# Performance work log

Hardware: AMD Instinct MI355X
Metric: run time of the kernel (lower is better)

## Reference

```python
import jax, jax.numpy as jnp
import numpy as np

N = 30000   # fluid particles
E = 480000  # edges
F = 4       # fluidFeatures (in channels)
P = 8       # RBF basis size per dim (dims=[8], 1D)
LAYERS = [32, 64, 64, 2]


def hat_basis(x, n):
    # 'linear' RBF: hat functions on n evenly spaced centers in [-1, 1]
    centers = jnp.linspace(-1.0, 1.0, n, dtype=x.dtype)
    spacing = 2.0 / (n - 1)
    return jnp.maximum(0.0, 1.0 - jnp.abs(x[:, None] - centers[None, :]) / spacing)  # [E, n]


def rbf_conv(x, fi, fj, d, W, b, mask, n_nodes):
    # x: [N, Cin]; d: [E, 1] clamped; W: [P, Cin, Cout]; b: [Cout]
    phi = hat_basis(d[:, 0], W.shape[0])      # [E, P]
    xj = x[fj]                                 # gather source features [E, Cin]
    msg = jnp.zeros((xj.shape[0], W.shape[2]), dtype=x.dtype)
    for p in range(W.shape[0]):                # small fixed P=8 loop keeps memory O(E*Cout)
        msg = msg + phi[:, p, None] * (xj @ W[p])
    msg = jnp.where(mask[:, None], msg, 0.0)   # centerIgnore: drop self edges fi==fj
    out = jax.ops.segment_sum(msg, fi, num_segments=n_nodes)  # scatter-reduce to targets
    return out + b


def _xavier(key, shape_in, shape_out):
    lim = float(np.sqrt(6.0 / (shape_in + shape_out)))
    return jax.random.uniform(key, (shape_in, shape_out), jnp.float32, -lim, lim)


def setup_inputs() -> dict:
    key = jax.random.key(0)
    ks = jax.random.split(key, 16)
    fluidFeatures = jax.random.normal(ks[0], (N, F), jnp.float32)
    fi = jax.random.randint(ks[1], (E,), 0, N)
    fj = jax.random.randint(ks[2], (E,), 0, N)
    distances = jax.random.normal(ks[3], (E, 1), jnp.float32)
    # conv channels: 4->32, 64->64, 64->64, 64->2
    cio = [(F, 32), (2 * 32, 64), (64, 64), (64, 2)]
    inp = {"fluidFeatures": fluidFeatures, "fi": fi, "fj": fj, "distances": distances}
    for li, (ci, co) in enumerate(cio):
        inp[f"cW{li}"] = jax.random.normal(ks[4 + li], (P, ci, co), jnp.float32) * (1.0 / np.sqrt(P * ci))
        inp[f"cb{li}"] = jnp.zeros((co,), jnp.float32)
        inp[f"fW{li}"] = _xavier(ks[8 + li], ci, co)   # stored [in, out]
        inp[f"fb{li}"] = jnp.zeros((co,), jnp.float32)
    return inp


def reference(fluidFeatures, fi, fj, distances,
              cW0, cb0, fW0, fb0, cW1, cb1, fW1, fb1,
              cW2, cb2, fW2, fb2, cW3, cb3, fW3, fb3):
    n_nodes = fluidFeatures.shape[0]
    mask = fi != fj                     # centerIgnore (mask instead of filter: jit-safe)
    d = jnp.clip(distances, -1.0, 1.0)

    conv0 = rbf_conv(fluidFeatures, fi, fj, d, cW0, cb0, mask, n_nodes)  # [N, 32]
    lin0 = fluidFeatures @ fW0 + fb0                                      # [N, 32]
    ans = jnp.concatenate([lin0, conv0], axis=1)                          # [N, 64]

    # i = 1: features[0]=32 != features[1]=64 -> no residual
    ansc = jax.nn.relu(ans)
    ans = rbf_conv(ansc, fi, fj, d, cW1, cb1, mask, n_nodes) + (ansc @ fW1 + fb1)
    # i = 2: features[1]==features[2]==64 and shapes match -> residual
    ansc = jax.nn.relu(ans)
    ans = rbf_conv(ansc, fi, fj, d, cW2, cb2, mask, n_nodes) + (ansc @ fW2 + fb2) + ans
    # i = 3: 64 -> 2, no residual
    ansc = jax.nn.relu(ans)
    ans = rbf_conv(ansc, fi, fj, d, cW3, cb3, mask, n_nodes) + (ansc @ fW3 + fb3)

    return ans  # dim == 1 (dims=[8]) -> no /128
```

## Files before the change

### kernel.cpp

```cpp
#include <hip/hip_runtime.h>


#define CAP 48

typedef __attribute__((ext_vector_type(8))) short short8;
typedef __attribute__((ext_vector_type(4))) short short4v;
typedef __attribute__((ext_vector_type(4))) float f32x4;

__device__ __forceinline__ short bf16s(float f) {
  unsigned u = __float_as_uint(f);
  return (short)((u + 0x7FFF + ((u >> 16) & 1)) >> 16);
}
__device__ __forceinline__ float b2f(unsigned short s) {
  return __uint_as_float(((unsigned)s) << 16);
}

__global__ void fill_prep(const float* __restrict__ dist,
                          const int* __restrict__ fi, const int* __restrict__ fj,
                          int* __restrict__ cnt, int* __restrict__ jw, int nE,
                          const float* __restrict__ cW1, const float* __restrict__ fW1,
                          const float* __restrict__ cW2, const float* __restrict__ fW2,
                          short* __restrict__ wt1, short* __restrict__ wt2,
                          int fillBlocks) {
  if ((int)blockIdx.x < fillBlocks) {
    int e = blockIdx.x * blockDim.x + threadIdx.x;
    if (e >= nE) return;
    int i = fi[e], j = fj[e];
    if (i == j) return;
    float d = fminf(1.0f, fmaxf(-1.0f, dist[e]));
    float u = (d + 1.0f) * 3.5f;
    int p = min((int)u, 6);
    float w0 = 1.0f - (u - (float)p);
    int wq = (int)(w0 * 16383.0f + 0.5f);
    int pos = atomicAdd(&cnt[i], 1);
    if (pos < CAP)
      jw[(size_t)i * CAP + pos] = j | (p << 15) | (wq << 18);
  } else {
    int idx = ((int)blockIdx.x - fillBlocks) * blockDim.x + threadIdx.x;
    if (idx >= 2 * 576 * 64) return;
    int sel = idx / (576 * 64);
    int r = idx - sel * (576 * 64);
    int col = r >> 6, ch = r & 63;
    const float* cW = sel ? cW2 : cW1;
    const float* fW = sel ? fW2 : fW1;
    float v;
    if (col < 512) {
      int p = col >> 6, co = col & 63;
      v = cW[((size_t)p * 64 + ch) * 64 + co];
    } else {
      v = fW[(size_t)ch * 64 + (col - 512)];
    }
    (sel ? wt2 : wt1)[(size_t)col * 64 + ch] = bf16s(v);
  }
}

__global__ __launch_bounds__(256) void layer0_kernel(
    const float* __restrict__ X,
    const int* __restrict__ cnt, const int* __restrict__ jw,
    const float* __restrict__ cW0,
    const float* __restrict__ cb0,
    const float* __restrict__ fW0,
    const float* __restrict__ fb0,
    unsigned short* __restrict__ ansc0, int n) {
  __shared__ float sW[1024];
  __shared__ float sF[128];
  __shared__ float sB[64];
  __shared__ float sacc[4][32];
  for (int idx = threadIdx.x; idx < 1024; idx += 256) sW[idx] = cW0[idx];
  for (int idx = threadIdx.x; idx < 128; idx += 256) sF[idx] = fW0[idx];
  if (threadIdx.x < 32) sB[threadIdx.x] = cb0[threadIdx.x];
  else if (threadIdx.x < 64) sB[threadIdx.x] = fb0[threadIdx.x - 32];
  const int w = threadIdx.x >> 6;
  const int lane = threadIdx.x & 63;
  const int i = blockIdx.x * 4 + w;
  const bool valid = (i < n);
  if (valid && lane < 32) sacc[w][lane] = 0.0f;
  __syncthreads();
  if (valid && lane < min(cnt[i], CAP)) {
    int v = jw[(size_t)i * CAP + lane];
    int j = v & 0x7FFF;
    int p = (v >> 15) & 7;
    float w0 = (float)((unsigned)v >> 18) * (1.0f / 16383.0f);
    float w1 = 1.0f - w0;
    float4 x = *(const float4*)(X + (size_t)j * 4);
    atomicAdd(&sacc[w][p * 4 + 0], w0 * x.x);
    atomicAdd(&sacc[w][p * 4 + 1], w0 * x.y);
    atomicAdd(&sacc[w][p * 4 + 2], w0 * x.z);
    atomicAdd(&sacc[w][p * 4 + 3], w0 * x.w);
    atomicAdd(&sacc[w][(p + 1) * 4 + 0], w1 * x.x);
    atomicAdd(&sacc[w][(p + 1) * 4 + 1], w1 * x.y);
    atomicAdd(&sacc[w][(p + 1) * 4 + 2], w1 * x.z);
    atomicAdd(&sacc[w][(p + 1) * 4 + 3], w1 * x.w);
  }
  __syncthreads();
  if (!valid) return;
  const float4 xi = *(const float4*)(X + (size_t)i * 4);
  float v;
  if (lane < 32) {
    v = sB[32 + lane];
    v = fmaf(xi.x, sF[0 * 32 + lane], v);
    v = fmaf(xi.y, sF[1 * 32 + lane], v);
    v = fmaf(xi.z, sF[2 * 32 + lane], v);
    v = fmaf(xi.w, sF[3 * 32 + lane], v);
  } else {
    const int cc = lane - 32;
    v = sB[cc];
    #pragma unroll
    for (int k = 0; k < 32; ++k)
      v = fmaf(sacc[w][k], sW[k * 32 + cc], v);
  }
  ansc0[(size_t)i * 64 + lane] = (unsigned short)bf16s(fmaxf(v, 0.0f));
}

__global__ __launch_bounds__(256) void gemm_ul(
    const unsigned short* __restrict__ Xb,
    const short* __restrict__ WTul,
    unsigned short* __restrict__ UL, int n) {
  __shared__ short sUL[16 * 584];
  const int lane = threadIdx.x & 63;
  const int w = threadIdx.x >> 6;
  const int mrow = lane & 15;
  const int quad = lane >> 4;
  const int nodeBase = blockIdx.x * 16;
  const int bnode = min(nodeBase + mrow, n - 1);
  const unsigned short* bBase = Xb + (size_t)bnode * 64 + quad * 8;
  short8 b0 = *(const short8*)(bBase);
  short8 b1 = *(const short8*)(bBase + 32);
  #pragma unroll
  for (int t = 0; t < 9; ++t) {
    const int ct = w * 9 + t;
    const short* aBase = WTul + (size_t)(ct * 16 + mrow) * 64 + quad * 8;
    short8 a0 = *(const short8*)(aBase);
    short8 a1 = *(const short8*)(aBase + 32);
    f32x4 acc = {0, 0, 0, 0};
    acc = __builtin_amdgcn_mfma_f32_16x16x32_bf16(a0, b0, acc, 0, 0, 0);
    acc = __builtin_amdgcn_mfma_f32_16x16x32_bf16(a1, b1, acc, 0, 0, 0);
    short4v pk;
    #pragma unroll
    for (int reg = 0; reg < 4; ++reg) pk[reg] = bf16s(acc[reg]);
    *(short4v*)(sUL + mrow * 584 + ct * 16 + quad * 4) = pk;
  }
  __syncthreads();
  const int r = threadIdx.x >> 4;
  const int c0 = threadIdx.x & 15;
  if (nodeBase + r < n) {
    unsigned short* dst = UL + (size_t)(nodeBase + r) * 576;
    #pragma unroll
    for (int chunk = c0; chunk < 72; chunk += 16)
      *(short8*)(dst + chunk * 8) = *(const short8*)(sUL + r * 584 + chunk * 8);
  }
}

template <bool HAS_RES, bool STORE_ANS, bool COMPUTE_T>
__global__ __launch_bounds__(256) void conv_gather(
    const unsigned short* __restrict__ UL,
    const int* __restrict__ cnt, const int* __restrict__ jw,
    const float* __restrict__ cb, const float* __restrict__ fb,
    const float* __restrict__ resid,
    const float* __restrict__ cW3,
    float* __restrict__ T,
    float* __restrict__ outAns,
    unsigned short* __restrict__ outAnsc, int n) {
  const int lane = threadIdx.x & 63;
  const int half = lane >> 5;
  const int pl = lane & 31;
  const int i = (blockIdx.x * blockDim.x + threadIdx.x) >> 6;
  if (i >= n) return;
  int rec = jw[(size_t)i * CAP + (lane < CAP ? lane : 0)];
  const int m = min(cnt[i], CAP);
  const unsigned short* ULrow = UL + (size_t)i * 576;
  const unsigned Lraw = ((const unsigned*)(ULrow + 512))[pl];
  float rv0 = 0.0f, rv1 = 0.0f;
  if (HAS_RES) {
    float2 rv = *(const float2*)(resid + (size_t)i * 64 + 2 * pl);
    rv0 = rv.x; rv1 = rv.y;
  }
  float accLo = 0.0f, accHi = 0.0f;
  for (int q0 = 0; q0 < m; q0 += 16) {
    unsigned raw[16];
    float w0s[16];
    #pragma unroll
    for (int k = 0; k < 16; ++k) {
      int v = __builtin_amdgcn_readlane(rec, q0 + k);
      int j = min(v & 0x7FFF, n - 1);
      int p = (v >> 15) & 7;
      w0s[k] = (float)((unsigned)v >> 18) * (1.0f / 16383.0f);
      raw[k] = ((const unsigned*)(UL + (size_t)j * 576 + p * 64))[lane];
    }
    #pragma unroll
    for (int k = 0; k < 16; ++k) {
      bool ok = (q0 + k < m);
      float w = half ? (1.0f - w0s[k]) : w0s[k];
      w = ok ? w : 0.0f;
      float lo = __uint_as_float(raw[k] << 16);
      float hi = __uint_as_float(raw[k] & 0xFFFF0000u);
      accLo = fmaf(w, lo, accLo);
      accHi = fmaf(w, hi, accHi);
    }
  }
  accLo += __shfl_xor(accLo, 32, 64);
  accHi += __shfl_xor(accHi, 32, 64);
  if (half == 0) {
    const int c0i = 2 * pl, c1i = c0i + 1;
    float L0 = __uint_as_float(Lraw << 16);
    float L1 = __uint_as_float(Lraw & 0xFFFF0000u);
    float o0 = accLo + L0 + cb[c0i] + fb[c0i] + rv0;
    float o1 = accHi + L1 + cb[c1i] + fb[c1i] + rv1;
    if (STORE_ANS)
      *(float2*)(outAns + (size_t)i * 64 + c0i) = make_float2(o0, o1);
    unsigned short xb0 = (unsigned short)bf16s(fmaxf(o0, 0.0f));
    unsigned short xb1 = (unsigned short)bf16s(fmaxf(o1, 0.0f));
    ((unsigned*)(outAnsc + (size_t)i * 64))[pl] = (unsigned)xb0 | ((unsigned)xb1 << 16);
    if (COMPUTE_T) {
      float x0 = b2f(xb0), x1 = b2f(xb1);
      float c[16];
      #pragma unroll
      for (int t = 0; t < 16; ++t) {
        const float* wrow = cW3 + ((size_t)(t >> 1) * 64) * 2 + (t & 1);
        c[t] = x0 * wrow[c0i * 2] + x1 * wrow[c1i * 2];
      }
      #pragma unroll
      for (int off = 16; off > 0; off >>= 1) {
        #pragma unroll
        for (int t = 0; t < 16; ++t) c[t] += __shfl_xor(c[t], off, 64);
      }
      if (pl == 0) {
        float* tr = T + (size_t)i * 16;
        #pragma unroll
        for (int t = 0; t < 16; ++t) tr[t] = c[t];
      }
    }
  }
}

__global__ __launch_bounds__(256, 4) void layer3_kernel(
    const unsigned short* __restrict__ Xb,
    const float* __restrict__ T,
    const int* __restrict__ cnt, const int* __restrict__ jw,
    const float* __restrict__ cb3, const float* __restrict__ fb3,
    const float* __restrict__ fW3,
    float* __restrict__ out, int n) {
  const int lane = threadIdx.x & 63;
  const int i = (blockIdx.x * blockDim.x + threadIdx.x) >> 6;
  if (i >= n) return;
  const int m = min(cnt[i], CAP);
  float c0 = 0.0f, c1 = 0.0f;
  if (lane < m) {
    int v = jw[(size_t)i * CAP + lane];
    int j = min(v & 0x7FFF, n - 1);
    int p = (v >> 15) & 7;
    float w0 = (float)((unsigned)v >> 18) * (1.0f / 16383.0f);
    float w1 = 1.0f - w0;
    const float* tb = T + (size_t)j * 16 + p * 2;
    float2 ta = *(const float2*)(tb);
    float2 tc = *(const float2*)(tb + 2);
    c0 = w0 * ta.x + w1 * tc.x;
    c1 = w0 * ta.y + w1 * tc.y;
  }
  float xi = b2f(Xb[(size_t)i * 64 + lane]);
  float2 fw = *(const float2*)(fW3 + lane * 2);
  c0 = fmaf(xi, fw.x, c0);
  c1 = fmaf(xi, fw.y, c1);
  #pragma unroll
  for (int off = 32; off > 0; off >>= 1) {
    c0 += __shfl_xor(c0, off, 64);
    c1 += __shfl_xor(c1, off, 64);
  }
  if (lane == 0) {
    out[(size_t)i * 2 + 0] = c0 + cb3[0] + fb3[0];
    out[(size_t)i * 2 + 1] = c1 + cb3[1] + fb3[1];
  }
}

extern "C" void kernel_launch(void* const* d_in, const int* in_sizes, int n_in,
                              void* d_out, int out_size, void* d_ws, size_t ws_size,
                              hipStream_t stream) {
  const float* X    = (const float*)d_in[0];
  const int*   fi   = (const int*)d_in[1];
  const int*   fj   = (const int*)d_in[2];
  const float* dist = (const float*)d_in[3];
  const float* cW0 = (const float*)d_in[4];  const float* cb0 = (const float*)d_in[5];
  const float* fW0 = (const float*)d_in[6];  const float* fb0 = (const float*)d_in[7];
  const float* cW1 = (const float*)d_in[8];  const float* cb1 = (const float*)d_in[9];
  const float* fW1 = (const float*)d_in[10]; const float* fb1 = (const float*)d_in[11];
  const float* cW2 = (const float*)d_in[12]; const float* cb2 = (const float*)d_in[13];
  const float* fW2 = (const float*)d_in[14]; const float* fb2 = (const float*)d_in[15];
  const float* cW3 = (const float*)d_in[16]; const float* cb3 = (const float*)d_in[17];
  const float* fW3 = (const float*)d_in[18]; const float* fb3 = (const float*)d_in[19];
  float* out = (float*)d_out;

  const int n  = in_sizes[0] / 4;
  const int nE = in_sizes[1];

  unsigned short* UL    = (unsigned short*)d_ws;
  unsigned short* ansc0 = UL + (size_t)n * 576;
  unsigned short* ansc1 = ansc0 + (size_t)n * 64;
  float*          ans1  = (float*)(ansc1 + (size_t)n * 64);
  unsigned short* ansc2 = ansc0;
  float* T     = ans1 + (size_t)n * 64;
  short* wtul1 = (short*)(T + (size_t)n * 16);
  short* wtul2 = wtul1 + 576 * 64;
  int*   jw    = (int*)(wtul2 + 576 * 64);
  int*   cnt   = jw + (size_t)n * CAP;

  hipMemsetAsync(cnt, 0, (size_t)n * sizeof(int), stream);
  const int fillBlocks = (nE + 255) / 256;
  const int prepBlocks = (2 * 576 * 64 + 255) / 256;
  fill_prep<<<fillBlocks + prepBlocks, 256, 0, stream>>>(
      dist, fi, fj, cnt, jw, nE, cW1, fW1, cW2, fW2, wtul1, wtul2, fillBlocks);

  layer0_kernel<<<(n + 3) / 4, 256, 0, stream>>>(X, cnt, jw,
                                                 cW0, cb0, fW0, fb0, ansc0, n);
  gemm_ul<<<(n + 15) / 16, 256, 0, stream>>>(ansc0, wtul1, UL, n);
  conv_gather<false, true, false><<<(n * 64 + 255) / 256, 256, 0, stream>>>(
      UL, cnt, jw, cb1, fb1, nullptr, nullptr, nullptr, ans1, ansc1, n);
  gemm_ul<<<(n + 15) / 16, 256, 0, stream>>>(ansc1, wtul2, UL, n);
  conv_gather<true, false, true><<<(n * 64 + 255) / 256, 256, 0, stream>>>(
      UL, cnt, jw, cb2, fb2, ans1, cW3, T, nullptr, ansc2, n);
  layer3_kernel<<<(n * 64 + 255) / 256, 256, 0, stream>>>(ansc2, T, cnt, jw,
                                                          cb3, fb3, fW3, out, n);
}
```

Measured before the change: 270.2 us.

## Fuse all stages into one persistent cooperative kernel with grid syncs

Replaces the memset and the six separate kernel launches with a single cooperative persistent kernel. It iterates over nodes and tiles with grid-stride loops and separates the phases with grid.sync(). This removes per-launch overhead and the memset. In exchange it adds grid-wide barrier costs, lowers occupancy through the fixed block count, and calls hipGetDeviceProperties and the occupancy query on every launch.

```diff
diff --git a/kernel.cpp b/kernel.cpp
--- a/kernel.cpp
+++ b/kernel.cpp
@@ -1,4 +1,7 @@
 #include <hip/hip_runtime.h>
+#include <hip/hip_cooperative_groups.h>
+
+namespace cg = cooperative_groups;
 
 
 #define CAP 48
@@ -15,34 +18,153 @@
   return __uint_as_float(((unsigned)s) << 16);
 }
 
-__global__ void fill_prep(const float* __restrict__ dist,
-                          const int* __restrict__ fi, const int* __restrict__ fj,
-                          int* __restrict__ cnt, int* __restrict__ jw, int nE,
-                          const float* __restrict__ cW1, const float* __restrict__ fW1,
-                          const float* __restrict__ cW2, const float* __restrict__ fW2,
-                          short* __restrict__ wt1, short* __restrict__ wt2,
-                          int fillBlocks) {
-  if ((int)blockIdx.x < fillBlocks) {
-    int e = blockIdx.x * blockDim.x + threadIdx.x;
-    if (e >= nE) return;
-    int i = fi[e], j = fj[e];
-    if (i == j) return;
-    float d = fminf(1.0f, fmaxf(-1.0f, dist[e]));
-    float u = (d + 1.0f) * 3.5f;
-    int p = min((int)u, 6);
-    float w0 = 1.0f - (u - (float)p);
-    int wq = (int)(w0 * 16383.0f + 0.5f);
-    int pos = atomicAdd(&cnt[i], 1);
-    if (pos < CAP)
-      jw[(size_t)i * CAP + pos] = j | (p << 15) | (wq << 18);
-  } else {
-    int idx = ((int)blockIdx.x - fillBlocks) * blockDim.x + threadIdx.x;
-    if (idx >= 2 * 576 * 64) return;
+struct MegaParams {
+  const float* X; const int* fi; const int* fj; const float* dist;
+  const float* cW0; const float* cb0; const float* fW0; const float* fb0;
+  const float* cW1; const float* cb1; const float* fW1; const float* fb1;
+  const float* cW2; const float* cb2; const float* fW2; const float* fb2;
+  const float* cW3; const float* cb3; const float* fW3; const float* fb3;
+  unsigned short* UL; unsigned short* ansc0; unsigned short* ansc1;
+  float* ans1; float* T; short* wt1; short* wt2; int* jw; int* cnt;
+  float* out; int n; int nE;
+};
+
+__device__ __forceinline__ void gemm_ul_phase(
+    const unsigned short* __restrict__ Xb, const short* __restrict__ WTul,
+    unsigned short* __restrict__ UL, int n, char* smemRaw) {
+  short* sUL = (short*)smemRaw;
+  const int lane = threadIdx.x & 63;
+  const int w = threadIdx.x >> 6;
+  const int mrow = lane & 15;
+  const int quad = lane >> 4;
+  for (int tile = blockIdx.x; tile * 16 < n; tile += gridDim.x) {
+    __syncthreads();
+    const int nodeBase = tile * 16;
+    const int bnode = min(nodeBase + mrow, n - 1);
+    const unsigned short* bBase = Xb + (size_t)bnode * 64 + quad * 8;
+    short8 b0 = *(const short8*)(bBase);
+    short8 b1 = *(const short8*)(bBase + 32);
+    #pragma unroll
+    for (int t = 0; t < 9; ++t) {
+      const int ct = w * 9 + t;
+      const short* aBase = WTul + (size_t)(ct * 16 + mrow) * 64 + quad * 8;
+      short8 a0 = *(const short8*)(aBase);
+      short8 a1 = *(const short8*)(aBase + 32);
+      f32x4 acc = {0, 0, 0, 0};
+      acc = __builtin_amdgcn_mfma_f32_16x16x32_bf16(a0, b0, acc, 0, 0, 0);
+      acc = __builtin_amdgcn_mfma_f32_16x16x32_bf16(a1, b1, acc, 0, 0, 0);
+      short4v pk;
+      #pragma unroll
+      for (int reg = 0; reg < 4; ++reg) pk[reg] = bf16s(acc[reg]);
+      *(short4v*)(sUL + mrow * 584 + ct * 16 + quad * 4) = pk;
+    }
+    __syncthreads();
+    const int r = threadIdx.x >> 4;
+    const int c0 = threadIdx.x & 15;
+    if (nodeBase + r < n) {
+      unsigned short* dst = UL + (size_t)(nodeBase + r) * 576;
+      #pragma unroll
+      for (int chunk = c0; chunk < 72; chunk += 16)
+        *(short8*)(dst + chunk * 8) = *(const short8*)(sUL + r * 584 + chunk * 8);
+    }
+  }
+}
+
+template <bool HAS_RES, bool STORE_ANS, bool COMPUTE_T>
+__device__ __forceinline__ void conv_phase(
+    const unsigned short* __restrict__ UL,
+    const int* __restrict__ cnt, const int* __restrict__ jw,
+    const float* __restrict__ cb, const float* __restrict__ fb,
+    const float* __restrict__ resid, const float* __restrict__ cW3,
+    float* __restrict__ T, float* __restrict__ outAns,
+    unsigned short* __restrict__ outAnsc, int n, int gwave, int NW) {
+  const int lane = threadIdx.x & 63;
+  const int half = lane >> 5;
+  const int pl = lane & 31;
+  const int c0i = 2 * pl, c1i = c0i + 1;
+  const float cbf0 = cb[c0i] + fb[c0i];
+  const float cbf1 = cb[c1i] + fb[c1i];
+  for (int i = gwave; i < n; i += NW) {
+    int rec = jw[(size_t)i * CAP + (lane < CAP ? lane : 0)];
+    const int m = min(cnt[i], CAP);
+    const unsigned Lraw = ((const unsigned*)(UL + (size_t)i * 576 + 512))[pl];
+    float rv0 = 0.0f, rv1 = 0.0f;
+    if (HAS_RES) {
+      float2 rv = *(const float2*)(resid + (size_t)i * 64 + 2 * pl);
+      rv0 = rv.x; rv1 = rv.y;
+    }
+    float accLo = 0.0f, accHi = 0.0f;
+    for (int q0 = 0; q0 < m; q0 += 16) {
+      unsigned raw[16];
+      float w0s[16];
+      #pragma unroll
+      for (int k = 0; k < 16; ++k) {
+        int v = __builtin_amdgcn_readlane(rec, q0 + k);
+        int j = min(v & 0x7FFF, n - 1);
+        int p = (v >> 15) & 7;
+        w0s[k] = (float)((unsigned)v >> 18) * (1.0f / 16383.0f);
+        raw[k] = ((const unsigned*)(UL + (size_t)j * 576 + p * 64))[lane];
+      }
+      #pragma unroll
+      for (int k = 0; k < 16; ++k) {
+        bool ok = (q0 + k < m);
+        float w = half ? (1.0f - w0s[k]) : w0s[k];
+        w = ok ? w : 0.0f;
+        accLo = fmaf(w, __uint_as_float(raw[k] << 16), accLo);
+        accHi = fmaf(w, __uint_as_float(raw[k] & 0xFFFF0000u), accHi);
+      }
+    }
+    accLo += __shfl_xor(accLo, 32, 64);
+    accHi += __shfl_xor(accHi, 32, 64);
+    if (half == 0) {
+      float o0 = accLo + __uint_as_float(Lraw << 16) + cbf0 + rv0;
+      float o1 = accHi + __uint_as_float(Lraw & 0xFFFF0000u) + cbf1 + rv1;
+      if (STORE_ANS)
+        *(float2*)(outAns + (size_t)i * 64 + c0i) = make_float2(o0, o1);
+      unsigned short xb0 = (unsigned short)bf16s(fmaxf(o0, 0.0f));
+      unsigned short xb1 = (unsigned short)bf16s(fmaxf(o1, 0.0f));
+      ((unsigned*)(outAnsc + (size_t)i * 64))[pl] = (unsigned)xb0 | ((unsigned)xb1 << 16);
+      if (COMPUTE_T) {
+        float x0 = b2f(xb0), x1 = b2f(xb1);
+        float c[16];
+        #pragma unroll
+        for (int t = 0; t < 16; ++t) {
+          const float* wrow = cW3 + ((size_t)(t >> 1) * 64) * 2 + (t & 1);
+          c[t] = x0 * wrow[c0i * 2] + x1 * wrow[c1i * 2];
+        }
+        #pragma unroll
+        for (int off = 16; off > 0; off >>= 1) {
+          #pragma unroll
+          for (int t = 0; t < 16; ++t) c[t] += __shfl_xor(c[t], off, 64);
+        }
+        if (pl == 0) {
+          float* tr = T + (size_t)i * 16;
+          #pragma unroll
+          for (int t = 0; t < 16; ++t) tr[t] = c[t];
+        }
+      }
+    }
+  }
+}
+
+__global__ __launch_bounds__(256, 4) void mega_kernel(MegaParams P) {
+  cg::grid_group grid = cg::this_grid();
+  __shared__ __align__(16) char smem[18688];
+  const int tid = (int)(blockIdx.x * blockDim.x + threadIdx.x);
+  const int NT = (int)(gridDim.x * blockDim.x);
+  const int lane = threadIdx.x & 63;
+  const int wIn = threadIdx.x >> 6;
+  const int gwave = tid >> 6;
+  const int NW = NT >> 6;
+  const int n = P.n;
+
+  for (int i = tid; i < n; i += NT) P.cnt[i] = 0;
+  for (int idx = tid; idx < 2 * 576 * 64; idx += NT) {
     int sel = idx / (576 * 64);
     int r = idx - sel * (576 * 64);
     int col = r >> 6, ch = r & 63;
-    const float* cW = sel ? cW2 : cW1;
-    const float* fW = sel ? fW2 : fW1;
+    const float* cW = sel ? P.cW2 : P.cW1;
+    const float* fW = sel ? P.fW2 : P.fW1;
     float v;
     if (col < 512) {
       int p = col >> 6, co = col & 63;
@@ -50,273 +172,174 @@
     } else {
       v = fW[(size_t)ch * 64 + (col - 512)];
     }
-    (sel ? wt2 : wt1)[(size_t)col * 64 + ch] = bf16s(v);
-  }
-}
-
-__global__ __launch_bounds__(256) void layer0_kernel(
-    const float* __restrict__ X,
-    const int* __restrict__ cnt, const int* __restrict__ jw,
-    const float* __restrict__ cW0,
-    const float* __restrict__ cb0,
-    const float* __restrict__ fW0,
-    const float* __restrict__ fb0,
-    unsigned short* __restrict__ ansc0, int n) {
-  __shared__ float sW[1024];
-  __shared__ float sF[128];
-  __shared__ float sB[64];
-  __shared__ float sacc[4][32];
-  for (int idx = threadIdx.x; idx < 1024; idx += 256) sW[idx] = cW0[idx];
-  for (int idx = threadIdx.x; idx < 128; idx += 256) sF[idx] = fW0[idx];
-  if (threadIdx.x < 32) sB[threadIdx.x] = cb0[threadIdx.x];
-  else if (threadIdx.x < 64) sB[threadIdx.x] = fb0[threadIdx.x - 32];
-  const int w = threadIdx.x >> 6;
-  const int lane = threadIdx.x & 63;
-  const int i = blockIdx.x * 4 + w;
-  const bool valid = (i < n);
-  if (valid && lane < 32) sacc[w][lane] = 0.0f;
-  __syncthreads();
-  if (valid && lane < min(cnt[i], CAP)) {
-    int v = jw[(size_t)i * CAP + lane];
-    int j = v & 0x7FFF;
-    int p = (v >> 15) & 7;
-    float w0 = (float)((unsigned)v >> 18) * (1.0f / 16383.0f);
-    float w1 = 1.0f - w0;
-    float4 x = *(const float4*)(X + (size_t)j * 4);
-    atomicAdd(&sacc[w][p * 4 + 0], w0 * x.x);
-    atomicAdd(&sacc[w][p * 4 + 1], w0 * x.y);
-    atomicAdd(&sacc[w][p * 4 + 2], w0 * x.z);
-    atomicAdd(&sacc[w][p * 4 + 3], w0 * x.w);
-    atomicAdd(&sacc[w][(p + 1) * 4 + 0], w1 * x.x);
-    atomicAdd(&sacc[w][(p + 1) * 4 + 1], w1 * x.y);
-    atomicAdd(&sacc[w][(p + 1) * 4 + 2], w1 * x.z);
-    atomicAdd(&sacc[w][(p + 1) * 4 + 3], w1 * x.w);
-  }
-  __syncthreads();
-  if (!valid) return;
-  const float4 xi = *(const float4*)(X + (size_t)i * 4);
-  float v;
-  if (lane < 32) {
-    v = sB[32 + lane];
-    v = fmaf(xi.x, sF[0 * 32 + lane], v);
-    v = fmaf(xi.y, sF[1 * 32 + lane], v);
-    v = fmaf(xi.z, sF[2 * 32 + lane], v);
-    v = fmaf(xi.w, sF[3 * 32 + lane], v);
-  } else {
-    const int cc = lane - 32;
-    v = sB[cc];
-    #pragma unroll
-    for (int k = 0; k < 32; ++k)
-      v = fmaf(sacc[w][k], sW[k * 32 + cc], v);
-  }
-  ansc0[(size_t)i * 64 + lane] = (unsigned short)bf16s(fmaxf(v, 0.0f));
-}
-
-__global__ __launch_bounds__(256) void gemm_ul(
-    const unsigned short* __restrict__ Xb,
-    const short* __restrict__ WTul,
-    unsigned short* __restrict__ UL, int n) {
-  __shared__ short sUL[16 * 584];
-  const int lane = threadIdx.x & 63;
-  const int w = threadIdx.x >> 6;
-  const int mrow = lane & 15;
-  const int quad = lane >> 4;
-  const int nodeBase = blockIdx.x * 16;
-  const int bnode = min(nodeBase + mrow, n - 1);
-  const unsigned short* bBase = Xb + (size_t)bnode * 64 + quad * 8;
-  short8 b0 = *(const short8*)(bBase);
-  short8 b1 = *(const short8*)(bBase + 32);
-  #pragma unroll
-  for (int t = 0; t < 9; ++t) {
-    const int ct = w * 9 + t;
-    const short* aBase = WTul + (size_t)(ct * 16 + mrow) * 64 + quad * 8;
-    short8 a0 = *(const short8*)(aBase);
-    short8 a1 = *(const short8*)(aBase + 32);
-    f32x4 acc = {0, 0, 0, 0};
-    acc = __builtin_amdgcn_mfma_f32_16x16x32_bf16(a0, b0, acc, 0, 0, 0);
-    acc = __builtin_amdgcn_mfma_f32_16x16x32_bf16(a1, b1, acc, 0, 0, 0);
-    short4v pk;
-    #pragma unroll
-    for (int reg = 0; reg < 4; ++reg) pk[reg] = bf16s(acc[reg]);
-    *(short4v*)(sUL + mrow * 584 + ct * 16 + quad * 4) = pk;
-  }
-  __syncthreads();
-  const int r = threadIdx.x >> 4;
-  const int c0 = threadIdx.x & 15;
-  if (nodeBase + r < n) {
-    unsigned short* dst = UL + (size_t)(nodeBase + r) * 576;
-    #pragma unroll
-    for (int chunk = c0; chunk < 72; chunk += 16)
-      *(short8*)(dst + chunk * 8) = *(const short8*)(sUL + r * 584 + chunk * 8);
-  }
-}
-
-template <bool HAS_RES, bool STORE_ANS, bool COMPUTE_T>
-__global__ __launch_bounds__(256) void conv_gather(
-    const unsigned short* __restrict__ UL,
-    const int* __restrict__ cnt, const int* __restrict__ jw,
-    const float* __restrict__ cb, const float* __restrict__ fb,
-    const float* __restrict__ resid,
-    const float* __restrict__ cW3,
-    float* __restrict__ T,
-    float* __restrict__ outAns,
-    unsigned short* __restrict__ outAnsc, int n) {
-  const int lane = threadIdx.x & 63;
-  const int half = lane >> 5;
-  const int pl = lane & 31;
-  const int i = (blockIdx.x * blockDim.x + threadIdx.x) >> 6;
-  if (i >= n) return;
-  int rec = jw[(size_t)i * CAP + (lane < CAP ? lane : 0)];
-  const int m = min(cnt[i], CAP);
-  const unsigned short* ULrow = UL + (size_t)i * 576;
-  const unsigned Lraw = ((const unsigned*)(ULrow + 512))[pl];
-  float rv0 = 0.0f, rv1 = 0.0f;
-  if (HAS_RES) {
-    float2 rv = *(const float2*)(resid + (size_t)i * 64 + 2 * pl);
-    rv0 = rv.x; rv1 = rv.y;
-  }
-  float accLo = 0.0f, accHi = 0.0f;
-  for (int q0 = 0; q0 < m; q0 += 16) {
-    unsigned raw[16];
-    float w0s[16];
-    #pragma unroll
-    for (int k = 0; k < 16; ++k) {
-      int v = __builtin_amdgcn_readlane(rec, q0 + k);
-      int j = min(v & 0x7FFF, n - 1);
-      int p = (v >> 15) & 7;
-      w0s[k] = (float)((unsigned)v >> 18) * (1.0f / 16383.0f);
-      raw[k] = ((const unsigned*)(UL + (size_t)j * 576 + p * 64))[lane];
-    }
-    #pragma unroll
-    for (int k = 0; k < 16; ++k) {
-      bool ok = (q0 + k < m);
-      float w = half ? (1.0f - w0s[k]) : w0s[k];
-      w = ok ? w : 0.0f;
-      float lo = __uint_as_float(raw[k] << 16);
-      float hi = __uint_as_float(raw[k] & 0xFFFF0000u);
-      accLo = fmaf(w, lo, accLo);
-      accHi = fmaf(w, hi, accHi);
-    }
-  }
-  accLo += __shfl_xor(accLo, 32, 64);
-  accHi += __shfl_xor(accHi, 32, 64);
-  if (half == 0) {
-    const int c0i = 2 * pl, c1i = c0i + 1;
-    float L0 = __uint_as_float(Lraw << 16);
-    float L1 = __uint_as_float(Lraw & 0xFFFF0000u);
-    float o0 = accLo + L0 + cb[c0i] + fb[c0i] + rv0;
-    float o1 = accHi + L1 + cb[c1i] + fb[c1i] + rv1;
-    if (STORE_ANS)
-      *(float2*)(outAns + (size_t)i * 64 + c0i) = make_float2(o0, o1);
-    unsigned short xb0 = (unsigned short)bf16s(fmaxf(o0, 0.0f));
-    unsigned short xb1 = (unsigned short)bf16s(fmaxf(o1, 0.0f));
-    ((unsigned*)(outAnsc + (size_t)i * 64))[pl] = (unsigned)xb0 | ((unsigned)xb1 << 16);
-    if (COMPUTE_T) {
-      float x0 = b2f(xb0), x1 = b2f(xb1);
-      float c[16];
-      #pragma unroll
-      for (int t = 0; t < 16; ++t) {
-        const float* wrow = cW3 + ((size_t)(t >> 1) * 64) * 2 + (t & 1);
-        c[t] = x0 * wrow[c0i * 2] + x1 * wrow[c1i * 2];
-      }
-      #pragma unroll
-      for (int off = 16; off > 0; off >>= 1) {
-        #pragma unroll
-        for (int t = 0; t < 16; ++t) c[t] += __shfl_xor(c[t], off, 64);
-      }
-      if (pl == 0) {
-        float* tr = T + (size_t)i * 16;
-        #pragma unroll
-        for (int t = 0; t < 16; ++t) tr[t] = c[t];
-      }
-    }
-  }
-}
-
-__global__ __launch_bounds__(256, 4) void layer3_kernel(
-    const unsigned short* __restrict__ Xb,
-    const float* __restrict__ T,
-    const int* __restrict__ cnt, const int* __restrict__ jw,
-    const float* __restrict__ cb3, const float* __restrict__ fb3,
-    const float* __restrict__ fW3,
-    float* __restrict__ out, int n) {
-  const int lane = threadIdx.x & 63;
-  const int i = (blockIdx.x * blockDim.x + threadIdx.x) >> 6;
-  if (i >= n) return;
-  const int m = min(cnt[i], CAP);
-  float c0 = 0.0f, c1 = 0.0f;
-  if (lane < m) {
-    int v = jw[(size_t)i * CAP + lane];
-    int j = min(v & 0x7FFF, n - 1);
-    int p = (v >> 15) & 7;
-    float w0 = (float)((unsigned)v >> 18) * (1.0f / 16383.0f);
-    float w1 = 1.0f - w0;
-    const float* tb = T + (size_t)j * 16 + p * 2;
-    float2 ta = *(const float2*)(tb);
-    float2 tc = *(const float2*)(tb + 2);
-    c0 = w0 * ta.x + w1 * tc.x;
-    c1 = w0 * ta.y + w1 * tc.y;
-  }
-  float xi = b2f(Xb[(size_t)i * 64 + lane]);
-  float2 fw = *(const float2*)(fW3 + lane * 2);
-  c0 = fmaf(xi, fw.x, c0);
-  c1 = fmaf(xi, fw.y, c1);
-  #pragma unroll
-  for (int off = 32; off > 0; off >>= 1) {
-    c0 += __shfl_xor(c0, off, 64);
-    c1 += __shfl_xor(c1, off, 64);
-  }
-  if (lane == 0) {
-    out[(size_t)i * 2 + 0] = c0 + cb3[0] + fb3[0];
-    out[(size_t)i * 2 + 1] = c1 + cb3[1] + fb3[1];
+    (sel ? P.wt2 : P.wt1)[(size_t)col * 64 + ch] = bf16s(v);
+  }
+  grid.sync();
+
+  for (int e = tid; e < P.nE; e += NT) {
+    int i = P.fi[e], j = P.fj[e];
+    if (i == j) continue;
+    float d = fminf(1.0f, fmaxf(-1.0f, P.dist[e]));
+    float u = (d + 1.0f) * 3.5f;
+    int p = min((int)u, 6);
+    float w0 = 1.0f - (u - (float)p);
+    int wq = (int)(w0 * 16383.0f + 0.5f);
+    int pos = atomicAdd(&P.cnt[i], 1);
+    if (pos < CAP)
+      P.jw[(size_t)i * CAP + pos] = j | (p << 15) | (wq << 18);
+  }
+  grid.sync();
+
+  {
+    float* sW = (float*)smem;
+    float* sF = sW + 1024;
+    float* sB = sF + 128;
+    float* sacc = sB + 64;
+    for (int idx = threadIdx.x; idx < 1024; idx += 256) sW[idx] = P.cW0[idx];
+    for (int idx = threadIdx.x; idx < 128; idx += 256) sF[idx] = P.fW0[idx];
+    if (threadIdx.x < 32) sB[threadIdx.x] = P.cb0[threadIdx.x];
+    else if (threadIdx.x < 64) sB[threadIdx.x] = P.fb0[threadIdx.x - 32];
+    for (int g4 = blockIdx.x; g4 * 4 < n; g4 += gridDim.x) {
+      const int i = g4 * 4 + wIn;
+      const bool valid = (i < n);
+      __syncthreads();
+      if (valid && lane < 32) sacc[wIn * 32 + lane] = 0.0f;
+      __syncthreads();
+      if (valid && lane < min(P.cnt[i], CAP)) {
+        int v = P.jw[(size_t)i * CAP + lane];
+        int j = v & 0x7FFF;
+        int p = (v >> 15) & 7;
+        float w0 = (float)((unsigned)v >> 18) * (1.0f / 16383.0f);
+        float w1 = 1.0f - w0;
+        float4 x = *(const float4*)(P.X + (size_t)j * 4);
+        atomicAdd(&sacc[wIn * 32 + p * 4 + 0], w0 * x.x);
+        atomicAdd(&sacc[wIn * 32 + p * 4 + 1], w0 * x.y);
+        atomicAdd(&sacc[wIn * 32 + p * 4 + 2], w0 * x.z);
+        atomicAdd(&sacc[wIn * 32 + p * 4 + 3], w0 * x.w);
+        atomicAdd(&sacc[wIn * 32 + (p + 1) * 4 + 0], w1 * x.x);
+        atomicAdd(&sacc[wIn * 32 + (p + 1) * 4 + 1], w1 * x.y);
+        atomicAdd(&sacc[wIn * 32 + (p + 1) * 4 + 2], w1 * x.z);
+        atomicAdd(&sacc[wIn * 32 + (p + 1) * 4 + 3], w1 * x.w);
+      }
+      __syncthreads();
+      if (valid) {
+        const float4 xi = *(const float4*)(P.X + (size_t)i * 4);
+        float v;
+        if (lane < 32) {
+          v = sB[32 + lane];
+          v = fmaf(xi.x, sF[0 * 32 + lane], v);
+          v = fmaf(xi.y, sF[1 * 32 + lane], v);
+          v = fmaf(xi.z, sF[2 * 32 + lane], v);
+          v = fmaf(xi.w, sF[3 * 32 + lane], v);
+        } else {
+          const int cc = lane - 32;
+          v = sB[cc];
+          #pragma unroll
+          for (int k = 0; k < 32; ++k)
+            v = fmaf(sacc[wIn * 32 + k], sW[k * 32 + cc], v);
+        }
+        P.ansc0[(size_t)i * 64 + lane] = (unsigned short)bf16s(fmaxf(v, 0.0f));
+      }
+    }
+  }
+  grid.sync();
+
+  gemm_ul_phase(P.ansc0, P.wt1, P.UL, n, smem);
+  grid.sync();
+  conv_phase<false, true, false>(P.UL, P.cnt, P.jw, P.cb1, P.fb1,
+                                 nullptr, nullptr, nullptr,
+                                 P.ans1, P.ansc1, n, gwave, NW);
+  grid.sync();
+  gemm_ul_phase(P.ansc1, P.wt2, P.UL, n, smem);
+  grid.sync();
+  conv_phase<true, false, true>(P.UL, P.cnt, P.jw, P.cb2, P.fb2,
+                                P.ans1, P.cW3, P.T,
+                                nullptr, P.ansc0, n, gwave, NW);
+  grid.sync();
+  {
+    const unsigned short* Xb = P.ansc0;
+    const float b3s0 = P.cb3[0] + P.fb3[0];
+    const float b3s1 = P.cb3[1] + P.fb3[1];
+    const float2 fw = *(const float2*)(P.fW3 + lane * 2);
+    for (int i = gwave; i < n; i += NW) {
+      const int m = min(P.cnt[i], CAP);
+      float c0 = 0.0f, c1 = 0.0f;
+      if (lane < m) {
+        int v = P.jw[(size_t)i * CAP + lane];
+        int j = min(v & 0x7FFF, n - 1);
+        int p = (v >> 15) & 7;
+        float w0 = (float)((unsigned)v >> 18) * (1.0f / 16383.0f);
+        float w1 = 1.0f - w0;
+        const float* tb = P.T + (size_t)j * 16 + p * 2;
+        float2 ta = *(const float2*)(tb);
+        float2 tc = *(const float2*)(tb + 2);
+        c0 = w0 * ta.x + w1 * tc.x;
+        c1 = w0 * ta.y + w1 * tc.y;
+      }
+      float xi = b2f(Xb[(size_t)i * 64 + lane]);
+      c0 = fmaf(xi, fw.x, c0);
+      c1 = fmaf(xi, fw.y, c1);
+      #pragma unroll
+      for (int off = 32; off > 0; off >>= 1) {
+        c0 += __shfl_xor(c0, off, 64);
+        c1 += __shfl_xor(c1, off, 64);
+      }
+      if (lane == 0) {
+        P.out[(size_t)i * 2 + 0] = c0 + b3s0;
+        P.out[(size_t)i * 2 + 1] = c1 + b3s1;
+      }
+    }
   }
 }
 
 extern "C" void kernel_launch(void* const* d_in, const int* in_sizes, int n_in,
                               void* d_out, int out_size, void* d_ws, size_t ws_size,
                               hipStream_t stream) {
-  const float* X    = (const float*)d_in[0];
-  const int*   fi   = (const int*)d_in[1];
-  const int*   fj   = (const int*)d_in[2];
-  const float* dist = (const float*)d_in[3];
-  const float* cW0 = (const float*)d_in[4];  const float* cb0 = (const float*)d_in[5];
-  const float* fW0 = (const float*)d_in[6];  const float* fb0 = (const float*)d_in[7];
-  const float* cW1 = (const float*)d_in[8];  const float* cb1 = (const float*)d_in[9];
-  const float* fW1 = (const float*)d_in[10]; const float* fb1 = (const float*)d_in[11];
-  const float* cW2 = (const float*)d_in[12]; const float* cb2 = (const float*)d_in[13];
-  const float* fW2 = (const float*)d_in[14]; const float* fb2 = (const float*)d_in[15];
-  const float* cW3 = (const float*)d_in[16]; const float* cb3 = (const float*)d_in[17];
-  const float* fW3 = (const float*)d_in[18]; const float* fb3 = (const float*)d_in[19];
-  float* out = (float*)d_out;
+  MegaParams P;
+  P.X   = (const float*)d_in[0];
+  P.fi  = (const int*)d_in[1];
+  P.fj  = (const int*)d_in[2];
+  P.dist = (const float*)d_in[3];
+  P.cW0 = (const float*)d_in[4];  P.cb0 = (const float*)d_in[5];
+  P.fW0 = (const float*)d_in[6];  P.fb0 = (const float*)d_in[7];
+  P.cW1 = (const float*)d_in[8];  P.cb1 = (const float*)d_in[9];
+  P.fW1 = (const float*)d_in[10]; P.fb1 = (const float*)d_in[11];
+  P.cW2 = (const float*)d_in[12]; P.cb2 = (const float*)d_in[13];
+  P.fW2 = (const float*)d_in[14]; P.fb2 = (const float*)d_in[15];
+  P.cW3 = (const float*)d_in[16]; P.cb3 = (const float*)d_in[17];
+  P.fW3 = (const float*)d_in[18]; P.fb3 = (const float*)d_in[19];
+  P.out = (float*)d_out;
 
   const int n  = in_sizes[0] / 4;
   const int nE = in_sizes[1];
+  P.n = n; P.nE = nE;
 
   unsigned short* UL    = (unsigned short*)d_ws;
   unsigned short* ansc0 = UL + (size_t)n * 576;
   unsigned short* ansc1 = ansc0 + (size_t)n * 64;
   float*          ans1  = (float*)(ansc1 + (size_t)n * 64);
-  unsigned short* ansc2 = ansc0;
   float* T     = ans1 + (size_t)n * 64;
-  short* wtul1 = (short*)(T + (size_t)n * 16);
-  short* wtul2 = wtul1 + 576 * 64;
-  int*   jw    = (int*)(wtul2 + 576 * 64);
+  short* wt1   = (short*)(T + (size_t)n * 16);
+  short* wt2   = wt1 + 576 * 64;
+  int*   jw    = (int*)(wt2 + 576 * 64);
   int*   cnt   = jw + (size_t)n * CAP;
-
-  hipMemsetAsync(cnt, 0, (size_t)n * sizeof(int), stream);
-  const int fillBlocks = (nE + 255) / 256;
-  const int prepBlocks = (2 * 576 * 64 + 255) / 256;
-  fill_prep<<<fillBlocks + prepBlocks, 256, 0, stream>>>(
-      dist, fi, fj, cnt, jw, nE, cW1, fW1, cW2, fW2, wtul1, wtul2, fillBlocks);
-
-  layer0_kernel<<<(n + 3) / 4, 256, 0, stream>>>(X, cnt, jw,
-                                                 cW0, cb0, fW0, fb0, ansc0, n);
-  gemm_ul<<<(n + 15) / 16, 256, 0, stream>>>(ansc0, wtul1, UL, n);
-  conv_gather<false, true, false><<<(n * 64 + 255) / 256, 256, 0, stream>>>(
-      UL, cnt, jw, cb1, fb1, nullptr, nullptr, nullptr, ans1, ansc1, n);
-  gemm_ul<<<(n + 15) / 16, 256, 0, stream>>>(ansc1, wtul2, UL, n);
-  conv_gather<true, false, true><<<(n * 64 + 255) / 256, 256, 0, stream>>>(
-      UL, cnt, jw, cb2, fb2, ans1, cW3, T, nullptr, ansc2, n);
-  layer3_kernel<<<(n * 64 + 255) / 256, 256, 0, stream>>>(ansc2, T, cnt, jw,
-                                                          cb3, fb3, fW3, out, n);
-}
+  P.UL = UL; P.ansc0 = ansc0; P.ansc1 = ansc1; P.ans1 = ans1;
+  P.T = T; P.wt1 = wt1; P.wt2 = wt2; P.jw = jw; P.cnt = cnt;
+
+  int perCU = 0;
+  if (hipOccupancyMaxActiveBlocksPerMultiprocessor(
+          &perCU, (const void*)mega_kernel, 256, 0) != hipSuccess || perCU < 1)
+    perCU = 2;
+  int numCU = 256;
+  hipDeviceProp_t prop;
+  int dev = 0;
+  if (hipGetDevice(&dev) == hipSuccess &&
+      hipGetDeviceProperties(&prop, dev) == hipSuccess)
+    numCU = prop.multiProcessorCount;
+  int blocks = perCU * numCU;
+  if (blocks > 4096) blocks = 4096;
+
+  void* args[] = { &P };
+  hipLaunchCooperativeKernel((const void*)mega_kernel, dim3(blocks), dim3(256),
+                             args, 0, stream);
+}
```

Result: slower. 749.3 us (+177.3%).
